# Kernel optimization log

Measured on AMD Instinct MI355X. Metric: run time of the kernel, lower is better.

## Reference

```python
import jax, jax.numpy as jnp
import numpy as np

B, L, H, P = 4, 4096, 1024, 256


def _bin_op(ei, ej):
    A_i, Bu_i = ei
    A_j, Bu_j = ej
    return (A_j * A_i, A_j * Bu_i + Bu_j)


def _s5(x, log_real, imag, B_real, B_imag, C_real, C_imag, D, log_Delta):
    Lam = jax.lax.complex(-jnp.exp(log_real), imag)                 # [P]
    B_tilde = jax.lax.complex(B_real, B_imag)                        # [P,H]
    C_tilde = jax.lax.complex(C_real, C_imag)                        # [H,P]
    Delta = jnp.exp(log_Delta)                                       # [P]
    Lambda_bar = jnp.exp(Lam * Delta)                                # [P]
    Lam_safe = jnp.where(jnp.abs(Lam) < 1e-6,
                         jnp.full_like(Lam, 1e-6), Lam)
    B_bar = ((Lambda_bar - 1.0) / Lam_safe)[:, None] * B_tilde       # [P,H]
    Bu = x.astype(jnp.complex64) @ B_bar.T                           # [B,L,P]
    La = jnp.broadcast_to(Lambda_bar[None, None, :], Bu.shape)
    _, xs = jax.lax.associative_scan(_bin_op, (La, Bu), axis=1)      # [B,L,P]
    ys = jnp.real(xs @ C_tilde.T) + D * x                            # [B,L,H]
    return jax.nn.gelu(ys, approximate=False)


def setup_inputs() -> dict:
    key = jax.random.key(0)
    ks = jax.random.split(key, 17)
    std_b = 1.0 / H ** 0.5
    std_c = 1.0 / P ** 0.5
    d = {"x": jax.random.normal(ks[0], (B, L, H), dtype=jnp.float32)}
    for i, pfx in enumerate(["fwd", "bwd"]):
        o = 1 + 8 * i
        d[pfx + "_log_real"] = jax.random.normal(ks[o], (P,)) * 0.5
        d[pfx + "_imag"] = jax.random.normal(ks[o + 1], (P,))
        d[pfx + "_B_real"] = jax.random.normal(ks[o + 2], (P, H)) * std_b
        d[pfx + "_B_imag"] = jax.random.normal(ks[o + 3], (P, H)) * std_b
        d[pfx + "_C_real"] = jax.random.normal(ks[o + 4], (H, P)) * std_c
        d[pfx + "_C_imag"] = jax.random.normal(ks[o + 5], (H, P)) * std_c
        d[pfx + "_D"] = jnp.ones((H,), dtype=jnp.float32)
        d[pfx + "_log_Delta"] = jnp.zeros((P,), dtype=jnp.float32)
    return d


def reference(x,
              fwd_log_real, fwd_imag, fwd_B_real, fwd_B_imag,
              fwd_C_real, fwd_C_imag, fwd_D, fwd_log_Delta,
              bwd_log_real, bwd_imag, bwd_B_real, bwd_B_imag,
              bwd_C_real, bwd_C_imag, bwd_D, bwd_log_Delta):
    y_f = _s5(x, fwd_log_real, fwd_imag, fwd_B_real, fwd_B_imag,
              fwd_C_real, fwd_C_imag, fwd_D, fwd_log_Delta)
    x_flip = jnp.flip(x, axis=1)
    y_b = _s5(x_flip, bwd_log_real, bwd_imag, bwd_B_real, bwd_B_imag,
              bwd_C_real, bwd_C_imag, bwd_D, bwd_log_Delta)
    return y_f + jnp.flip(y_b, axis=1)
```

## Files before the change

kernel.cpp:

```cpp
#include <hip/hip_runtime.h>
#include <math.h>


typedef short bf16x8 __attribute__((ext_vector_type(8)));
typedef float f32x4 __attribute__((ext_vector_type(4)));
typedef unsigned short u16x8 __attribute__((ext_vector_type(8)));

__device__ __forceinline__ unsigned short f2bf(float f) {
  union { float f; unsigned int u; } v; v.f = f;
  unsigned int r = (v.u + 0x7FFFu + ((v.u >> 16) & 1u)) >> 16;
  return (unsigned short)r;
}
__device__ __forceinline__ float bf2f(unsigned short s) {
  union { unsigned int u; float f; } v; v.u = ((unsigned int)s) << 16;
  return v.f;
}
__device__ __forceinline__ float gelu_fast(float v) {
  const float u = 1.5957691216057308f * fmaf(0.044715f * v, v * v, v);
  return v / (1.f + __expf(-u));
}
__device__ __forceinline__ void gload16(const unsigned short* g, void* l) {
  __builtin_amdgcn_global_load_lds(
      (const __attribute__((address_space(1))) void*)g,
      (__attribute__((address_space(3))) void*)l, 16, 0, 0);
}

__global__ __launch_bounds__(256) void cast_prep_kernel(
    const float* __restrict__ x, unsigned short* __restrict__ xbf,
    const float* __restrict__ flr, const float* __restrict__ fim,
    const float* __restrict__ fBr, const float* __restrict__ fBi,
    const float* __restrict__ fCr, const float* __restrict__ fCi,
    const float* __restrict__ flD,
    const float* __restrict__ blr, const float* __restrict__ bim,
    const float* __restrict__ bBr, const float* __restrict__ bBi,
    const float* __restrict__ bCr, const float* __restrict__ bCi,
    const float* __restrict__ blD,
    unsigned short* __restrict__ W, unsigned short* __restrict__ CmT,
    float4* __restrict__ lamp) {
  const int tid = threadIdx.x;
  if (blockIdx.x < 8192) {
    const size_t i = (size_t)blockIdx.x * 256 + tid;
    const float4* xv = (const float4*)x;
    float4 a = xv[2 * i], b = xv[2 * i + 1];
    u16x8 r;
    r[0] = f2bf(a.x); r[1] = f2bf(a.y); r[2] = f2bf(a.z); r[3] = f2bf(a.w);
    r[4] = f2bf(b.x); r[5] = f2bf(b.y); r[6] = f2bf(b.z); r[7] = f2bf(b.w);
    *(u16x8*)(xbf + 8 * i) = r;
    return;
  }
  const int bid = blockIdx.x - 8192;
  if (bid < 512) {
    const int dir = bid >> 8, p = bid & 255;
    const float* lr_ = dir ? blr : flr;
    const float* im_ = dir ? bim : fim;
    const float* lD_ = dir ? blD : flD;
    const float* Br_ = dir ? bBr : fBr;
    const float* Bi_ = dir ? bBi : fBi;
    const float Lre = -expf(lr_[p]);
    const float Lim = im_[p];
    const float Dl = expf(lD_[p]);
    const float ar = Lre * Dl, ai = Lim * Dl;
    const float er = expf(ar);
    const float lre = er * cosf(ai), lim = er * sinf(ai);
    const float e64 = expf(64.f * ar);
    const float l64re = e64 * cosf(64.f * ai), l64im = e64 * sinf(64.f * ai);
    float sre = Lre, sim = Lim;
    if (sqrtf(Lre * Lre + Lim * Lim) < 1e-6f) { sre = 1e-6f; sim = 0.f; }
    const float den = sre * sre + sim * sim;
    const float fre = ((lre - 1.f) * sre + lim * sim) / den;
    const float fi2 = (lim * sre - (lre - 1.f) * sim) / den;
    if (tid == 0) lamp[dir * 256 + p] = make_float4(lre, lim, l64re, l64im);
    const size_t rowR = (size_t)(dir * 512 + 2 * p) * 1024;
    const size_t rowI = rowR + 1024;
    for (int h = tid; h < 1024; h += 256) {
      const float Br = Br_[p * 1024 + h], Bi = Bi_[p * 1024 + h];
      W[rowR + h] = f2bf(fre * Br - fi2 * Bi);
      W[rowI + h] = f2bf(fre * Bi + fi2 * Br);
    }
  } else {
    const int h = bid - 512;
    for (int k = tid; k < 1024; k += 256) {
      const int dir = k >> 9, within = k & 511;
      const int p = within >> 1, comp = within & 1;
      const float* C = comp ? (dir ? bCi : fCi) : (dir ? bCr : fCr);
      float v = C[(size_t)h * 256 + p];
      if (comp) v = -v;
      CmT[(size_t)h * 1024 + k] = f2bf(v);
    }
  }
}

#define G1_STAGE(BUF, KT)                                                      \
  {                                                                            \
    const int k0 = (KT) << 6;                                                  \
    _Pragma("unroll") for (int i = 0; i < 4; ++i) {                            \
      const int r = (i << 6) + tr;                                             \
      const int o = ((BUF) << 15) + (i << 13) + (tid << 4);                    \
      gload16(xbf + (size_t)(m0 + r) * 1024 + (k0 + csw), (char*)As + o);      \
      gload16(W + (size_t)(n0 + r) * 1024 + (k0 + csw), (char*)Bs + o);        \
    }                                                                          \
  }

#define G1_COMPUTE(BUF, ACC)                                                   \
  {                                                                            \
    const int bo = (BUF) << 14;                            \
    bf16x8 bF[4][2];                                                           \
    _Pragma("unroll") for (int n4 = 0; n4 < 4; ++n4)                           \
        _Pragma("unroll") for (int kk2 = 0; kk2 < 2; ++kk2) {                  \
      const int row = (wn << 6) + (n4 << 4) + fr;                              \
      bF[n4][kk2] =                                                            \
          *(const bf16x8*)&Bs[bo + row * 64 + (((kk2 << 5) + ks) ^ sw)];       \
    }                                                                          \
    _Pragma("unroll") for (int ph = 0; ph < 4; ++ph) {                         \
      bf16x8 aF[2][2];                                                         \
      _Pragma("unroll") for (int mf2 = 0; mf2 < 2; ++mf2)                      \
          _Pragma("unroll") for (int kk2 = 0; kk2 < 2; ++kk2) {                \
        const int row = (wm << 7) + (((ph << 1) + mf2) << 4) + fr;             \
        aF[mf2][kk2] =                                                         \
            *(const bf16x8*)&As[bo + row * 64 + (((kk2 << 5) + ks) ^ sw)];     \
      }                                                                        \
      __builtin_amdgcn_s_setprio(1);                                           \
      _Pragma("unroll") for (int mf2 = 0; mf2 < 2; ++mf2)                      \
          _Pragma("unroll") for (int n4 = 0; n4 < 4; ++n4)                     \
              _Pragma("unroll") for (int kk2 = 0; kk2 < 2; ++kk2)              \
                  ACC[(ph << 1) + mf2][n4] =                                   \
                      __builtin_amdgcn_mfma_f32_16x16x32_bf16(                 \
                          aF[mf2][kk2], bF[n4][kk2], ACC[(ph << 1) + mf2][n4], \
                          0, 0, 0);                                            \
      __builtin_amdgcn_s_setprio(0);                                           \
    }                                                                          \
  }

__global__ __launch_bounds__(512, 2) void gemm1_kernel(
    const unsigned short* __restrict__ xbf, const unsigned short* __restrict__ W,
    unsigned short* __restrict__ Zb) {
  __shared__ unsigned short As[2 * 256 * 64];
  __shared__ unsigned short Bs[2 * 256 * 64];
  const int tid = threadIdx.x;
  const int lane = tid & 63;
  const int w = tid >> 6;
  const int wm = w >> 2, wn = w & 3;
  const int fr = lane & 15;
  const int ks = (lane >> 4) << 3;
  const int sw = (fr & 7) << 3;
  const int tr = tid >> 3;
  const int csw = ((tid & 7) ^ (tr & 7)) << 3;
  const int bsw = ((blockIdx.x & 7) << 5) + (blockIdx.x >> 3);
  const int nt = bsw & 3, mt = bsw >> 2;
  const int m0 = mt << 8, n0 = nt << 8;

  f32x4 acc[8][4] = {};

  G1_STAGE(0, 0);
  int cur = 0;
  for (int kt = 0; kt < 15; ++kt) {
    G1_STAGE(cur ^ 1, kt + 1);
    asm volatile("s_waitcnt vmcnt(8)" ::: "memory");
    __builtin_amdgcn_sched_barrier(0);
    __builtin_amdgcn_s_barrier();
    __builtin_amdgcn_sched_barrier(0);
    G1_COMPUTE(cur, acc);
    __builtin_amdgcn_sched_barrier(0);
    __builtin_amdgcn_s_barrier();
    __builtin_amdgcn_sched_barrier(0);
    cur ^= 1;
  }
  __syncthreads();
  G1_COMPUTE(cur, acc);

  const int rb = (lane >> 4) << 2;
#pragma unroll
  for (int mf = 0; mf < 8; ++mf)
#pragma unroll
    for (int n4 = 0; n4 < 4; ++n4) {
      const size_t gn = n0 + (wn << 6) + (n4 << 4) + fr;
#pragma unroll
      for (int r = 0; r < 4; ++r) {
        const size_t gm = m0 + (wm << 7) + (mf << 4) + rb + r;
        Zb[gm * 1024 + gn] = f2bf(acc[mf][n4][r]);
      }
    }
}

__global__ __launch_bounds__(256) void scanP_kernel(
    const unsigned int* __restrict__ Zp, const float4* __restrict__ lamp,
    float2* __restrict__ part) {
  const int p = threadIdx.x;
  const int k = blockIdx.x & 63;
  const int s = blockIdx.x >> 6;
  const int dir = s & 1, b = s >> 1;
  const float4 lp = lamp[dir * 256 + p];
  const float lre = lp.x, lim = lp.y;
  const size_t col = (size_t)dir * 256 + p;
  const size_t mbase = (size_t)b * 4096 + (size_t)k * 64;
  float sre = 0.f, sim = 0.f;
  if (dir == 0) {
    for (int i = 0; i < 64; ++i) {
      const unsigned int u = Zp[(mbase + i) * 512 + col];
      const float nr = fmaf(lre, sre, fmaf(-lim, sim, bf2f((unsigned short)u)));
      const float ni = fmaf(lre, sim, fmaf(lim, sre, bf2f((unsigned short)(u >> 16))));
      sre = nr; sim = ni;
    }
  } else {
    for (int i = 63; i >= 0; --i) {
      const unsigned int u = Zp[(mbase + i) * 512 + col];
      const float nr = fmaf(lre, sre, fmaf(-lim, sim, bf2f((unsigned short)u)));
      const float ni = fmaf(lre, sim, fmaf(lim, sre, bf2f((unsigned short)(u >> 16))));
      sre = nr; sim = ni;
    }
  }
  part[(size_t)(s * 64 + k) * 256 + p] = make_float2(sre, sim);
}

__global__ __launch_bounds__(256) void scanF_kernel(
    const unsigned int* __restrict__ Zp, const float4* __restrict__ lamp,
    const float2* __restrict__ part, unsigned int* __restrict__ xsbf) {
  const int p = threadIdx.x;
  const int k = blockIdx.x & 63;
  const int s = blockIdx.x >> 6;
  const int dir = s & 1, b = s >> 1;
  const float4 lp = lamp[dir * 256 + p];
  const float lre = lp.x, lim = lp.y, wr64 = lp.z, wi64 = lp.w;
  const size_t col = (size_t)dir * 256 + p;
  const size_t mbase = (size_t)b * 4096 + (size_t)k * 64;

  float cr = 0.f, ci = 0.f, wr = 1.f, wi = 0.f;
  if (dir == 0) {
    for (int j = k - 1; j >= 0; --j) {
      const float2 S = part[(size_t)(s * 64 + j) * 256 + p];
      cr = fmaf(wr, S.x, fmaf(-wi, S.y, cr));
      ci = fmaf(wr, S.y, fmaf(wi, S.x, ci));
      const float t = wr * wr64 - wi * wi64;
      wi = wr * wi64 + wi * wr64; wr = t;
    }
  } else {
    for (int j = k + 1; j < 64; ++j) {
      const float2 S = part[(size_t)(s * 64 + j) * 256 + p];
      cr = fmaf(wr, S.x, fmaf(-wi, S.y, cr));
      ci = fmaf(wr, S.y, fmaf(wi, S.x, ci));
      const float t = wr * wr64 - wi * wi64;
      wi = wr * wi64 + wi * wr64; wr = t;
    }
  }

  float sre = cr, sim = ci;
  if (dir == 0) {
    for (int i = 0; i < 64; ++i) {
      const size_t idx = (mbase + i) * 512 + col;
      const unsigned int u = Zp[idx];
      const float nr = fmaf(lre, sre, fmaf(-lim, sim, bf2f((unsigned short)u)));
      const float ni = fmaf(lre, sim, fmaf(lim, sre, bf2f((unsigned short)(u >> 16))));
      sre = nr; sim = ni;
      xsbf[idx] = (unsigned int)f2bf(sre) | ((unsigned int)f2bf(sim) << 16);
    }
  } else {
    for (int i = 63; i >= 0; --i) {
      const size_t idx = (mbase + i) * 512 + col;
      const unsigned int u = Zp[idx];
      const float nr = fmaf(lre, sre, fmaf(-lim, sim, bf2f((unsigned short)u)));
      const float ni = fmaf(lre, sim, fmaf(lim, sre, bf2f((unsigned short)(u >> 16))));
      sre = nr; sim = ni;
      xsbf[idx] = (unsigned int)f2bf(sre) | ((unsigned int)f2bf(sim) << 16);
    }
  }
}

#define GEMM_STAGE(BUF, KT, APTR, BPTR)                                        \
  {                                                                            \
    const int k0 = (KT) << 6;                                                  \
    _Pragma("unroll") for (int i = 0; i < 4; ++i) {                            \
      const int r = (i << 5) + tr;                                             \
      const int o = ((BUF) << 14) + (i << 12) + (tid << 4);                    \
      gload16(APTR + (size_t)(m0 + r) * 1024 + (k0 + csw), (char*)As + o);     \
      gload16(BPTR + (size_t)(n0 + r) * 1024 + (k0 + csw), (char*)Bs + o);     \
    }                                                                          \
  }

#define GEMM_COMPUTE(BUF, ACC)                                                 \
  {                                                                            \
    const int bo = (BUF) << 13;               \
    _Pragma("unroll") for (int kk = 0; kk < 64; kk += 32) {                    \
      bf16x8 af[4], bf_[4];                                                    \
      _Pragma("unroll") for (int m4 = 0; m4 < 4; ++m4) {                       \
        const int row = (wm << 6) + (m4 << 4) + fr;                            \
        af[m4] = *(const bf16x8*)&As[bo + row * 64 + ((kk + ks) ^ sw)];        \
      }                                                                        \
      _Pragma("unroll") for (int n4 = 0; n4 < 4; ++n4) {                       \
        const int row = (wn << 6) + (n4 << 4) + fr;                            \
        bf_[n4] = *(const bf16x8*)&Bs[bo + row * 64 + ((kk + ks) ^ sw)];       \
      }                                                                        \
      _Pragma("unroll") for (int m4 = 0; m4 < 4; ++m4)                         \
          _Pragma("unroll") for (int n4 = 0; n4 < 4; ++n4)                     \
              ACC[m4][n4] = __builtin_amdgcn_mfma_f32_16x16x32_bf16(           \
                  af[m4], bf_[n4], ACC[m4][n4], 0, 0, 0);                      \
    }                                                                          \
  }

#define PIPE_PUBLISH8()                                                        \
  asm volatile("s_waitcnt vmcnt(8)" ::: "memory");                             \
  __builtin_amdgcn_sched_barrier(0);                                           \
  __builtin_amdgcn_s_barrier();                                                \
  __builtin_amdgcn_sched_barrier(0);

#define PIPE_CLOSE()                                                           \
  __builtin_amdgcn_sched_barrier(0);                                           \
  __builtin_amdgcn_s_barrier();                                                \
  __builtin_amdgcn_sched_barrier(0);

__global__ __launch_bounds__(256, 2) void gemm2_kernel(
    const unsigned short* __restrict__ A2, const unsigned short* __restrict__ CmT,
    const unsigned short* __restrict__ xbf, const float* __restrict__ Df,
    const float* __restrict__ Db, float* __restrict__ out) {
  __shared__ unsigned short As[2 * 128 * 64];
  __shared__ unsigned short Bs[2 * 128 * 64];
  const int tid = threadIdx.x;
  const int lane = tid & 63;
  const int w = tid >> 6;
  const int wm = w >> 1, wn = w & 1;
  const int fr = lane & 15;
  const int ks = (lane >> 4) << 3;
  const int sw = (fr & 7) << 3;
  const int tr = tid >> 3;
  const int csw = ((tid & 7) ^ (tr & 7)) << 3;
  const int bsw = ((blockIdx.x & 7) << 7) + (blockIdx.x >> 3);
  const int nt = bsw & 7, mt = bsw >> 3;
  const int m0 = mt << 7, n0 = nt << 7;

  f32x4 accf[4][4] = {};
  f32x4 accb[4][4] = {};

  GEMM_STAGE(0, 0, A2, CmT);
  int cur = 0;
#pragma unroll
  for (int kt = 0; kt < 8; ++kt) {
    GEMM_STAGE(cur ^ 1, kt + 1, A2, CmT);
    PIPE_PUBLISH8();
    GEMM_COMPUTE(cur, accf);
    PIPE_CLOSE();
    cur ^= 1;
  }
#pragma unroll
  for (int kt = 8; kt < 15; ++kt) {
    GEMM_STAGE(cur ^ 1, kt + 1, A2, CmT);
    PIPE_PUBLISH8();
    GEMM_COMPUTE(cur, accb);
    PIPE_CLOSE();
    cur ^= 1;
  }
  __syncthreads();
  GEMM_COMPUTE(cur, accb);

  const int rb = (lane >> 4) << 2;
#pragma unroll
  for (int n4 = 0; n4 < 4; ++n4) {
    const size_t gn = n0 + (wn << 6) + (n4 << 4) + fr;
    const float dfv = Df[gn], dbv = Db[gn];
#pragma unroll
    for (int m4 = 0; m4 < 4; ++m4) {
#pragma unroll
      for (int r = 0; r < 4; ++r) {
        const size_t gm = m0 + (wm << 6) + (m4 << 4) + rb + r;
        const float xv = bf2f(xbf[gm * 1024 + gn]);
        out[gm * 1024 + gn] = gelu_fast(accf[m4][n4][r] + dfv * xv) +
                              gelu_fast(accb[m4][n4][r] + dbv * xv);
      }
    }
  }
}

extern "C" void kernel_launch(void* const* d_in, const int* in_sizes, int n_in,
                              void* d_out, int out_size, void* d_ws, size_t ws_size,
                              hipStream_t stream) {
  const float* x = (const float*)d_in[0];
  const float* flr = (const float*)d_in[1];
  const float* fim = (const float*)d_in[2];
  const float* fBr = (const float*)d_in[3];
  const float* fBi = (const float*)d_in[4];
  const float* fCr = (const float*)d_in[5];
  const float* fCi = (const float*)d_in[6];
  const float* fD  = (const float*)d_in[7];
  const float* flD = (const float*)d_in[8];
  const float* blr = (const float*)d_in[9];
  const float* bim = (const float*)d_in[10];
  const float* bBr = (const float*)d_in[11];
  const float* bBi = (const float*)d_in[12];
  const float* bCr = (const float*)d_in[13];
  const float* bCi = (const float*)d_in[14];
  const float* bD  = (const float*)d_in[15];
  const float* blD = (const float*)d_in[16];

  char* ws = (char*)d_ws;
  unsigned short* xbf  = (unsigned short*)(ws);
  unsigned short* W    = (unsigned short*)(ws + 33554432);
  unsigned short* CmT  = (unsigned short*)(ws + 35651584);
  unsigned short* Zb   = (unsigned short*)(ws + 37748736);
  unsigned short* xsbf = (unsigned short*)(ws + 71303168);
  float4*         lamp = (float4*)(ws + 104857600);
  float2*         part = (float2*)(ws + 104865792);

  cast_prep_kernel<<<9728, 256, 0, stream>>>(
      x, xbf, flr, fim, fBr, fBi, fCr, fCi, flD,
      blr, bim, bBr, bBi, bCr, bCi, blD, W, CmT, lamp);
  gemm1_kernel<<<256, 512, 0, stream>>>(xbf, W, Zb);
  scanP_kernel<<<512, 256, 0, stream>>>((unsigned int*)Zb, lamp, part);
  scanF_kernel<<<512, 256, 0, stream>>>((unsigned int*)Zb, lamp, part,
                                        (unsigned int*)xsbf);
  gemm2_kernel<<<1024, 256, 0, stream>>>(xsbf, CmT, xbf, fD, bD, (float*)d_out);
}
```

Measured before the change: 145.1 us.

## Enlarge gemm2 tiles to 256x256 with single accumulator and bf16 stash

The output GEMM moves from 128x128 tiles with 256 threads to 256x256 tiles with 512 threads, reusing the gemm1 staging and pipeline macros. To fit the larger tile in registers, it keeps one accumulator set. After the forward-direction K half it applies GELU, packs the result into a bf16 register stash and zeroes the accumulator before the backward half. Each byte staged in LDS now feeds more MFMA work. The cost is an extra bf16 rounding of the forward branch, a mid-loop epilogue, higher register pressure, and only 256 blocks in the grid.

```diff
diff --git a/kernel.cpp b/kernel.cpp
--- a/kernel.cpp
+++ b/kernel.cpp
@@ -90,16 +90,27 @@
   }
 }
 
-#define G1_STAGE(BUF, KT)                                                      \
+#define G256_STAGE(BUF, KT, APTR, BPTR)                                        \
   {                                                                            \
     const int k0 = (KT) << 6;                                                  \
     _Pragma("unroll") for (int i = 0; i < 4; ++i) {                            \
       const int r = (i << 6) + tr;                                             \
       const int o = ((BUF) << 15) + (i << 13) + (tid << 4);                    \
-      gload16(xbf + (size_t)(m0 + r) * 1024 + (k0 + csw), (char*)As + o);      \
-      gload16(W + (size_t)(n0 + r) * 1024 + (k0 + csw), (char*)Bs + o);        \
+      gload16(APTR + (size_t)(m0 + r) * 1024 + (k0 + csw), (char*)As + o);     \
+      gload16(BPTR + (size_t)(n0 + r) * 1024 + (k0 + csw), (char*)Bs + o);     \
     }                                                                          \
   }
+
+#define PIPE_PUBLISH8()                                                        \
+  asm volatile("s_waitcnt vmcnt(8)" ::: "memory");                             \
+  __builtin_amdgcn_sched_barrier(0);                                           \
+  __builtin_amdgcn_s_barrier();                                                \
+  __builtin_amdgcn_sched_barrier(0);
+
+#define PIPE_CLOSE()                                                           \
+  __builtin_amdgcn_sched_barrier(0);                                           \
+  __builtin_amdgcn_s_barrier();                                                \
+  __builtin_amdgcn_sched_barrier(0);
 
 #define G1_COMPUTE(BUF, ACC)                                                   \
   {                                                                            \
@@ -131,6 +142,34 @@
     }                                                                          \
   }
 
+#define G2_COMPUTE(BUF, ACC)                                                   \
+  {                                                                            \
+    const int bo = (BUF) << 14;                                                \
+    _Pragma("unroll") for (int kk2 = 0; kk2 < 2; ++kk2) {                      \
+      bf16x8 bF[4];                                                            \
+      _Pragma("unroll") for (int n4 = 0; n4 < 4; ++n4) {                       \
+        const int row = (wn << 6) + (n4 << 4) + fr;                            \
+        bF[n4] =                                                               \
+            *(const bf16x8*)&Bs[bo + row * 64 + (((kk2 << 5) + ks) ^ sw)];     \
+      }                                                                        \
+      _Pragma("unroll") for (int ph = 0; ph < 4; ++ph) {                       \
+        bf16x8 aF[2];                                                          \
+        _Pragma("unroll") for (int mf2 = 0; mf2 < 2; ++mf2) {                  \
+          const int row = (wm << 7) + (((ph << 1) + mf2) << 4) + fr;           \
+          aF[mf2] =                                                            \
+              *(const bf16x8*)&As[bo + row * 64 + (((kk2 << 5) + ks) ^ sw)];   \
+        }                                                                      \
+        __builtin_amdgcn_s_setprio(1);                                         \
+        _Pragma("unroll") for (int mf2 = 0; mf2 < 2; ++mf2)                    \
+            _Pragma("unroll") for (int n4 = 0; n4 < 4; ++n4)                   \
+                ACC[(ph << 1) + mf2][n4] =                                     \
+                    __builtin_amdgcn_mfma_f32_16x16x32_bf16(                   \
+                        aF[mf2], bF[n4], ACC[(ph << 1) + mf2][n4], 0, 0, 0);   \
+        __builtin_amdgcn_s_setprio(0);                                         \
+      }                                                                        \
+    }                                                                          \
+  }
+
 __global__ __launch_bounds__(512, 2) void gemm1_kernel(
     const unsigned short* __restrict__ xbf, const unsigned short* __restrict__ W,
     unsigned short* __restrict__ Zb) {
@@ -151,18 +190,13 @@
 
   f32x4 acc[8][4] = {};
 
-  G1_STAGE(0, 0);
+  G256_STAGE(0, 0, xbf, W);
   int cur = 0;
   for (int kt = 0; kt < 15; ++kt) {
-    G1_STAGE(cur ^ 1, kt + 1);
-    asm volatile("s_waitcnt vmcnt(8)" ::: "memory");
-    __builtin_amdgcn_sched_barrier(0);
-    __builtin_amdgcn_s_barrier();
-    __builtin_amdgcn_sched_barrier(0);
+    G256_STAGE(cur ^ 1, kt + 1, xbf, W);
+    PIPE_PUBLISH8();
     G1_COMPUTE(cur, acc);
-    __builtin_amdgcn_sched_barrier(0);
-    __builtin_amdgcn_s_barrier();
-    __builtin_amdgcn_sched_barrier(0);
+    PIPE_CLOSE();
     cur ^= 1;
   }
   __syncthreads();
@@ -265,107 +299,93 @@
   }
 }
 
-#define GEMM_STAGE(BUF, KT, APTR, BPTR)                                        \
-  {                                                                            \
-    const int k0 = (KT) << 6;                                                  \
-    _Pragma("unroll") for (int i = 0; i < 4; ++i) {                            \
-      const int r = (i << 5) + tr;                                             \
-      const int o = ((BUF) << 14) + (i << 12) + (tid << 4);                    \
-      gload16(APTR + (size_t)(m0 + r) * 1024 + (k0 + csw), (char*)As + o);     \
-      gload16(BPTR + (size_t)(n0 + r) * 1024 + (k0 + csw), (char*)Bs + o);     \
-    }                                                                          \
-  }
-
-#define GEMM_COMPUTE(BUF, ACC)                                                 \
-  {                                                                            \
-    const int bo = (BUF) << 13;               \
-    _Pragma("unroll") for (int kk = 0; kk < 64; kk += 32) {                    \
-      bf16x8 af[4], bf_[4];                                                    \
-      _Pragma("unroll") for (int m4 = 0; m4 < 4; ++m4) {                       \
-        const int row = (wm << 6) + (m4 << 4) + fr;                            \
-        af[m4] = *(const bf16x8*)&As[bo + row * 64 + ((kk + ks) ^ sw)];        \
-      }                                                                        \
-      _Pragma("unroll") for (int n4 = 0; n4 < 4; ++n4) {                       \
-        const int row = (wn << 6) + (n4 << 4) + fr;                            \
-        bf_[n4] = *(const bf16x8*)&Bs[bo + row * 64 + ((kk + ks) ^ sw)];       \
-      }                                                                        \
-      _Pragma("unroll") for (int m4 = 0; m4 < 4; ++m4)                         \
-          _Pragma("unroll") for (int n4 = 0; n4 < 4; ++n4)                     \
-              ACC[m4][n4] = __builtin_amdgcn_mfma_f32_16x16x32_bf16(           \
-                  af[m4], bf_[n4], ACC[m4][n4], 0, 0, 0);                      \
-    }                                                                          \
-  }
-
-#define PIPE_PUBLISH8()                                                        \
-  asm volatile("s_waitcnt vmcnt(8)" ::: "memory");                             \
-  __builtin_amdgcn_sched_barrier(0);                                           \
-  __builtin_amdgcn_s_barrier();                                                \
-  __builtin_amdgcn_sched_barrier(0);
-
-#define PIPE_CLOSE()                                                           \
-  __builtin_amdgcn_sched_barrier(0);                                           \
-  __builtin_amdgcn_s_barrier();                                                \
-  __builtin_amdgcn_sched_barrier(0);
-
-__global__ __launch_bounds__(256, 2) void gemm2_kernel(
+__global__ __launch_bounds__(512, 2) void gemm2_kernel(
     const unsigned short* __restrict__ A2, const unsigned short* __restrict__ CmT,
     const unsigned short* __restrict__ xbf, const float* __restrict__ Df,
     const float* __restrict__ Db, float* __restrict__ out) {
-  __shared__ unsigned short As[2 * 128 * 64];
-  __shared__ unsigned short Bs[2 * 128 * 64];
+  __shared__ unsigned short As[2 * 256 * 64];
+  __shared__ unsigned short Bs[2 * 256 * 64];
   const int tid = threadIdx.x;
   const int lane = tid & 63;
   const int w = tid >> 6;
-  const int wm = w >> 1, wn = w & 1;
+  const int wm = w >> 2, wn = w & 3;
   const int fr = lane & 15;
   const int ks = (lane >> 4) << 3;
   const int sw = (fr & 7) << 3;
   const int tr = tid >> 3;
   const int csw = ((tid & 7) ^ (tr & 7)) << 3;
-  const int bsw = ((blockIdx.x & 7) << 7) + (blockIdx.x >> 3);
-  const int nt = bsw & 7, mt = bsw >> 3;
-  const int m0 = mt << 7, n0 = nt << 7;
-
-  f32x4 accf[4][4] = {};
-  f32x4 accb[4][4] = {};
-
-  GEMM_STAGE(0, 0, A2, CmT);
+  const int bsw = ((blockIdx.x & 7) << 5) + (blockIdx.x >> 3);
+  const int nt = bsw & 3, mt = bsw >> 2;
+  const int m0 = mt << 8, n0 = nt << 8;
+  const int rb = (lane >> 4) << 2;
+
+  f32x4 acc[8][4] = {};
+  unsigned int stash[8][4][2];
+
+  G256_STAGE(0, 0, A2, CmT);
   int cur = 0;
 #pragma unroll
-  for (int kt = 0; kt < 8; ++kt) {
-    GEMM_STAGE(cur ^ 1, kt + 1, A2, CmT);
+  for (int kt = 0; kt < 7; ++kt) {
+    G256_STAGE(cur ^ 1, kt + 1, A2, CmT);
     PIPE_PUBLISH8();
-    GEMM_COMPUTE(cur, accf);
+    G2_COMPUTE(cur, acc);
     PIPE_CLOSE();
     cur ^= 1;
   }
+  G256_STAGE(cur ^ 1, 8, A2, CmT);
+  PIPE_PUBLISH8();
+  G2_COMPUTE(cur, acc);
+#pragma unroll
+  for (int mf = 0; mf < 8; ++mf)
+#pragma unroll
+    for (int n4 = 0; n4 < 4; ++n4) {
+      const size_t gn = n0 + (wn << 6) + (n4 << 4) + fr;
+      const float dfv = Df[gn];
+#pragma unroll
+      for (int pr = 0; pr < 2; ++pr) {
+        const size_t gm0 = m0 + (wm << 7) + (mf << 4) + rb + 2 * pr;
+        const float x0 = bf2f(xbf[gm0 * 1024 + gn]);
+        const float x1 = bf2f(xbf[(gm0 + 1) * 1024 + gn]);
+        const float g0 = gelu_fast(acc[mf][n4][2 * pr] + dfv * x0);
+        const float g1 = gelu_fast(acc[mf][n4][2 * pr + 1] + dfv * x1);
+        stash[mf][n4][pr] =
+            (unsigned int)f2bf(g0) | ((unsigned int)f2bf(g1) << 16);
+      }
+      acc[mf][n4] = (f32x4){0.f, 0.f, 0.f, 0.f};
+    }
+  PIPE_CLOSE();
+  cur ^= 1;
 #pragma unroll
   for (int kt = 8; kt < 15; ++kt) {
-    GEMM_STAGE(cur ^ 1, kt + 1, A2, CmT);
+    G256_STAGE(cur ^ 1, kt + 1, A2, CmT);
     PIPE_PUBLISH8();
-    GEMM_COMPUTE(cur, accb);
+    G2_COMPUTE(cur, acc);
     PIPE_CLOSE();
     cur ^= 1;
   }
   __syncthreads();
-  GEMM_COMPUTE(cur, accb);
-
-  const int rb = (lane >> 4) << 2;
-#pragma unroll
-  for (int n4 = 0; n4 < 4; ++n4) {
-    const size_t gn = n0 + (wn << 6) + (n4 << 4) + fr;
-    const float dfv = Df[gn], dbv = Db[gn];
-#pragma unroll
-    for (int m4 = 0; m4 < 4; ++m4) {
-#pragma unroll
-      for (int r = 0; r < 4; ++r) {
-        const size_t gm = m0 + (wm << 6) + (m4 << 4) + rb + r;
-        const float xv = bf2f(xbf[gm * 1024 + gn]);
-        out[gm * 1024 + gn] = gelu_fast(accf[m4][n4][r] + dfv * xv) +
-                              gelu_fast(accb[m4][n4][r] + dbv * xv);
+  G2_COMPUTE(cur, acc);
+
+#pragma unroll
+  for (int mf = 0; mf < 8; ++mf)
+#pragma unroll
+    for (int n4 = 0; n4 < 4; ++n4) {
+      const size_t gn = n0 + (wn << 6) + (n4 << 4) + fr;
+      const float dbv = Db[gn];
+#pragma unroll
+      for (int pr = 0; pr < 2; ++pr) {
+        const unsigned int st = stash[mf][n4][pr];
+        const size_t gm0 = m0 + (wm << 7) + (mf << 4) + rb + 2 * pr;
+        const float x0 = bf2f(xbf[gm0 * 1024 + gn]);
+        const float x1 = bf2f(xbf[(gm0 + 1) * 1024 + gn]);
+        out[gm0 * 1024 + gn] =
+            bf2f((unsigned short)st) +
+            gelu_fast(acc[mf][n4][2 * pr] + dbv * x0);
+        out[(gm0 + 1) * 1024 + gn] =
+            bf2f((unsigned short)(st >> 16)) +
+            gelu_fast(acc[mf][n4][2 * pr + 1] + dbv * x1);
       }
     }
-  }
 }
 
 extern "C" void kernel_launch(void* const* d_in, const int* in_sizes, int n_in,
@@ -405,5 +425,5 @@
   scanP_kernel<<<512, 256, 0, stream>>>((unsigned int*)Zb, lamp, part);
   scanF_kernel<<<512, 256, 0, stream>>>((unsigned int*)Zb, lamp, part,
                                         (unsigned int*)xsbf);
-  gemm2_kernel<<<1024, 256, 0, stream>>>(xsbf, CmT, xbf, fD, bD, (float*)d_out);
-}
+  gemm2_kernel<<<256, 512, 0, stream>>>(xsbf, CmT, xbf, fD, bD, (float*)d_out);
+}
```

Result: slower. 322.7 us (+122.5%).

## Split gemm1 tile loads into half-tiles interleaved with MFMA phases

Applied to the files above, without the earlier changes.

Restructures the gemm1 main loop so the A and B tiles are each loaded as two 128-row halves into separate LDS buffers. The loads for the next k-step are issued between the four MFMA phases of the current step, using finer vmcnt waits and a mid-iteration barrier in place of one bulk prefetch per step. The aim is to spread global-to-LDS traffic across the compute and overlap it better, in the style of an HipKittens-like 8-wave ping-pong. In exchange the synchronisation gets more complex and hand-set vmcnt counts risk races if they are wrong. Separately, gemm2 gets a variable rename and its pipeline macros move, with no behaviour change there.

```diff
diff --git a/kernel.cpp b/kernel.cpp
--- a/kernel.cpp
+++ b/kernel.cpp
@@ -90,52 +90,50 @@
   }
 }
 
-#define G1_STAGE(BUF, KT)                                                      \
+#define G1_SA(DBUF, H, KT)                                                     \
   {                                                                            \
-    const int k0 = (KT) << 6;                                                  \
-    _Pragma("unroll") for (int i = 0; i < 4; ++i) {                            \
-      const int r = (i << 6) + tr;                                             \
-      const int o = ((BUF) << 15) + (i << 13) + (tid << 4);                    \
-      gload16(xbf + (size_t)(m0 + r) * 1024 + (k0 + csw), (char*)As + o);      \
-      gload16(W + (size_t)(n0 + r) * 1024 + (k0 + csw), (char*)Bs + o);        \
+    _Pragma("unroll") for (int i = 0; i < 2; ++i) {                            \
+      const int rh = ((H) << 7) + (i << 6) + tr;                               \
+      const int o = ((((DBUF) << 1) | (H)) << 14) + (i << 13) + (tid << 4);    \
+      gload16(xbf + (size_t)(m0 + rh) * 1024 + ((KT) << 6) + csw,              \
+              (char*)As + o);                                                  \
     }                                                                          \
   }
-
-#define G1_COMPUTE(BUF, ACC)                                                   \
+#define G1_SB(DBUF, H, KT)                                                     \
   {                                                                            \
-    const int bo = (BUF) << 14;                            \
-    bf16x8 bF[4][2];                                                           \
-    _Pragma("unroll") for (int n4 = 0; n4 < 4; ++n4)                           \
+    _Pragma("unroll") for (int i = 0; i < 2; ++i) {                            \
+      const int rh = ((H) << 7) + (i << 6) + tr;                               \
+      const int o = ((((DBUF) << 1) | (H)) << 14) + (i << 13) + (tid << 4);    \
+      gload16(W + (size_t)(n0 + rh) * 1024 + ((KT) << 6) + csw,                \
+              (char*)Bs + o);                                                  \
+    }                                                                          \
+  }
+
+#define G1_PHASE(PH, D, ACC)                                                   \
+  {                                                                            \
+    bf16x8 aF[2][2];                                                           \
+    _Pragma("unroll") for (int mf2 = 0; mf2 < 2; ++mf2)                        \
         _Pragma("unroll") for (int kk2 = 0; kk2 < 2; ++kk2) {                  \
-      const int row = (wn << 6) + (n4 << 4) + fr;                              \
-      bF[n4][kk2] =                                                            \
-          *(const bf16x8*)&Bs[bo + row * 64 + (((kk2 << 5) + ks) ^ sw)];       \
+      const int rowh = ((PH) << 5) + (mf2 << 4) + fr;                          \
+      aF[mf2][kk2] = *(const bf16x8*)&As[((((D) << 1) | wm) << 13) +           \
+                                         rowh * 64 + (((kk2 << 5) + ks) ^ sw)];\
     }                                                                          \
-    _Pragma("unroll") for (int ph = 0; ph < 4; ++ph) {                         \
-      bf16x8 aF[2][2];                                                         \
-      _Pragma("unroll") for (int mf2 = 0; mf2 < 2; ++mf2)                      \
-          _Pragma("unroll") for (int kk2 = 0; kk2 < 2; ++kk2) {                \
-        const int row = (wm << 7) + (((ph << 1) + mf2) << 4) + fr;             \
-        aF[mf2][kk2] =                                                         \
-            *(const bf16x8*)&As[bo + row * 64 + (((kk2 << 5) + ks) ^ sw)];     \
-      }                                                                        \
-      __builtin_amdgcn_s_setprio(1);                                           \
-      _Pragma("unroll") for (int mf2 = 0; mf2 < 2; ++mf2)                      \
-          _Pragma("unroll") for (int n4 = 0; n4 < 4; ++n4)                     \
-              _Pragma("unroll") for (int kk2 = 0; kk2 < 2; ++kk2)              \
-                  ACC[(ph << 1) + mf2][n4] =                                   \
-                      __builtin_amdgcn_mfma_f32_16x16x32_bf16(                 \
-                          aF[mf2][kk2], bF[n4][kk2], ACC[(ph << 1) + mf2][n4], \
-                          0, 0, 0);                                            \
-      __builtin_amdgcn_s_setprio(0);                                           \
-    }                                                                          \
+    __builtin_amdgcn_s_setprio(1);                                             \
+    _Pragma("unroll") for (int mf2 = 0; mf2 < 2; ++mf2)                        \
+        _Pragma("unroll") for (int n4 = 0; n4 < 4; ++n4)                       \
+            _Pragma("unroll") for (int kk2 = 0; kk2 < 2; ++kk2)                \
+                ACC[((PH) << 1) + mf2][n4] =                                   \
+                    __builtin_amdgcn_mfma_f32_16x16x32_bf16(                   \
+                        aF[mf2][kk2], bF[n4][kk2], ACC[((PH) << 1) + mf2][n4], \
+                        0, 0, 0);                                              \
+    __builtin_amdgcn_s_setprio(0);                                             \
   }
 
 __global__ __launch_bounds__(512, 2) void gemm1_kernel(
     const unsigned short* __restrict__ xbf, const unsigned short* __restrict__ W,
     unsigned short* __restrict__ Zb) {
-  __shared__ unsigned short As[2 * 256 * 64];
-  __shared__ unsigned short Bs[2 * 256 * 64];
+  __shared__ unsigned short As[4 * 128 * 64];
+  __shared__ unsigned short Bs[4 * 128 * 64];
   const int tid = threadIdx.x;
   const int lane = tid & 63;
   const int w = tid >> 6;
@@ -151,22 +149,42 @@
 
   f32x4 acc[8][4] = {};
 
-  G1_STAGE(0, 0);
-  int cur = 0;
-  for (int kt = 0; kt < 15; ++kt) {
-    G1_STAGE(cur ^ 1, kt + 1);
-    asm volatile("s_waitcnt vmcnt(8)" ::: "memory");
+  G1_SB(0, 0, 0); G1_SB(0, 1, 0); G1_SA(0, 0, 0); G1_SA(0, 1, 0);
+
+  for (int kt = 0; kt < 16; ++kt) {
+    const int d = kt & 1, dn = d ^ 1;
+    bf16x8 bF[4][2];
+    asm volatile("s_waitcnt vmcnt(1)" ::: "memory");
     __builtin_amdgcn_sched_barrier(0);
     __builtin_amdgcn_s_barrier();
+    asm volatile("" ::: "memory");
     __builtin_amdgcn_sched_barrier(0);
-    G1_COMPUTE(cur, acc);
+    if (kt < 15) G1_SB(dn, 0, kt + 1);
+#pragma unroll
+    for (int n4 = 0; n4 < 4; ++n4)
+#pragma unroll
+      for (int kk2 = 0; kk2 < 2; ++kk2) {
+        const int rowh = ((wn & 1) << 6) + (n4 << 4) + fr;
+        bF[n4][kk2] = *(const bf16x8*)&Bs[(((d << 1) | (wn >> 1)) << 13) +
+                                          rowh * 64 + (((kk2 << 5) + ks) ^ sw)];
+      }
+    G1_PHASE(0, d, acc);
+    if (kt < 15) G1_SB(dn, 1, kt + 1);
+    G1_PHASE(1, d, acc);
+    if (kt < 15) {
+      asm volatile("s_waitcnt vmcnt(4)" ::: "memory");
+    } else {
+      asm volatile("s_waitcnt vmcnt(0)" ::: "memory");
+    }
     __builtin_amdgcn_sched_barrier(0);
     __builtin_amdgcn_s_barrier();
+    asm volatile("" ::: "memory");
     __builtin_amdgcn_sched_barrier(0);
-    cur ^= 1;
-  }
-  __syncthreads();
-  G1_COMPUTE(cur, acc);
+    if (kt < 15) G1_SA(dn, 0, kt + 1);
+    G1_PHASE(2, d, acc);
+    if (kt < 15) G1_SA(dn, 1, kt + 1);
+    G1_PHASE(3, d, acc);
+  }
 
   const int rb = (lane >> 4) << 2;
 #pragma unroll
@@ -269,12 +287,23 @@
   {                                                                            \
     const int k0 = (KT) << 6;                                                  \
     _Pragma("unroll") for (int i = 0; i < 4; ++i) {                            \
-      const int r = (i << 5) + tr;                                             \
+      const int r = (i << 5) + tr2;                                            \
       const int o = ((BUF) << 14) + (i << 12) + (tid << 4);                    \
       gload16(APTR + (size_t)(m0 + r) * 1024 + (k0 + csw), (char*)As + o);     \
       gload16(BPTR + (size_t)(n0 + r) * 1024 + (k0 + csw), (char*)Bs + o);     \
     }                                                                          \
   }
+
+#define PIPE_PUBLISH8()                                                        \
+  asm volatile("s_waitcnt vmcnt(8)" ::: "memory");                             \
+  __builtin_amdgcn_sched_barrier(0);                                           \
+  __builtin_amdgcn_s_barrier();                                                \
+  __builtin_amdgcn_sched_barrier(0);
+
+#define PIPE_CLOSE()                                                           \
+  __builtin_amdgcn_sched_barrier(0);                                           \
+  __builtin_amdgcn_s_barrier();                                                \
+  __builtin_amdgcn_sched_barrier(0);
 
 #define GEMM_COMPUTE(BUF, ACC)                                                 \
   {                                                                            \
@@ -296,17 +325,6 @@
     }                                                                          \
   }
 
-#define PIPE_PUBLISH8()                                                        \
-  asm volatile("s_waitcnt vmcnt(8)" ::: "memory");                             \
-  __builtin_amdgcn_sched_barrier(0);                                           \
-  __builtin_amdgcn_s_barrier();                                                \
-  __builtin_amdgcn_sched_barrier(0);
-
-#define PIPE_CLOSE()                                                           \
-  __builtin_amdgcn_sched_barrier(0);                                           \
-  __builtin_amdgcn_s_barrier();                                                \
-  __builtin_amdgcn_sched_barrier(0);
-
 __global__ __launch_bounds__(256, 2) void gemm2_kernel(
     const unsigned short* __restrict__ A2, const unsigned short* __restrict__ CmT,
     const unsigned short* __restrict__ xbf, const float* __restrict__ Df,
@@ -320,8 +338,8 @@
   const int fr = lane & 15;
   const int ks = (lane >> 4) << 3;
   const int sw = (fr & 7) << 3;
-  const int tr = tid >> 3;
-  const int csw = ((tid & 7) ^ (tr & 7)) << 3;
+  const int tr2 = tid >> 3;
+  const int csw = ((tid & 7) ^ (tr2 & 7)) << 3;
   const int bsw = ((blockIdx.x & 7) << 7) + (blockIdx.x >> 3);
   const int nt = bsw & 7, mt = bsw >> 3;
   const int m0 = mt << 7, n0 = nt << 7;
```

Result: slower. 150.6 us (+3.8%).
